# Kernel tuning notes

Measured on AMD Instinct MI355X. Metric: run time of the kernel, lower is better.

## Reference

```python
import jax, jax.numpy as jnp
import numpy as np

B, I, J, WIDTH, NH = 8, 1024, 1024, 512, 8
HD = WIDTH // NH
SCALE = WIDTH ** (-0.5)  # NOTE: original scales by width**-0.5, not head_dim**-0.5


def setup_inputs() -> dict:
    key = jax.random.key(0)
    ks = jax.random.split(key, 7)
    return {
        "q": jax.random.normal(ks[0], (B, I, WIDTH), dtype=jnp.float32),
        "k": jax.random.normal(ks[1], (B, J, WIDTH), dtype=jnp.float32),
        "v": jax.random.normal(ks[2], (B, J, WIDTH), dtype=jnp.float32),
        "Wq": jax.random.normal(ks[3], (WIDTH, WIDTH), dtype=jnp.float32) * (WIDTH ** -0.5),
        "Wk": jax.random.normal(ks[4], (WIDTH, WIDTH), dtype=jnp.float32) * (WIDTH ** -0.5),
        "Wv": jax.random.normal(ks[5], (WIDTH, WIDTH), dtype=jnp.float32) * (WIDTH ** -0.5),
        "Wo": jax.random.normal(ks[6], (WIDTH, WIDTH), dtype=jnp.float32) * (WIDTH ** -0.5),
    }


def reference(q, k, v, Wq, Wk, Wv, Wo):
    b, i, _ = q.shape
    j = k.shape[1]
    # Linear(bias=False): y = x @ W.T
    qh = (q @ Wq.T).reshape(b, NH, i, HD)  # faithful to torch .view(b, n, i, d) (no transpose)
    kh = (k @ Wk.T).reshape(b, NH, j, HD)
    vh = (v @ Wv.T).reshape(b, NH, j, HD)
    attn_score = jnp.einsum('bnid,bnjd->bnij', qh, kh) * SCALE
    attn_weight = jax.nn.softmax(attn_score, axis=3)
    # drop_prob = 0.0 -> dropout is identity
    x = jnp.einsum('bnij,bnjd->bnid', attn_weight, vh)
    x = x.transpose(0, 2, 1, 3).reshape(b, i, NH * HD)  # b n i d -> b i (n d)
    x = x @ Wo.T
    return (x, attn_weight)
```

## Files before the change

kernel.cpp:

```cpp
#include <hip/hip_runtime.h>
#include <hip/hip_bf16.h>


typedef __hip_bfloat16 bf16;
typedef __attribute__((ext_vector_type(8))) short bf16x8;
typedef __attribute__((ext_vector_type(4))) float f32x4;

#define BATCH 8
#define SEQ   1024
#define WIDTH 512
#define NHEAD 8
#define HD    64
#define SCALE_F 0.044194173824159216f

static __device__ __forceinline__ unsigned short f2bf(float x) {
  union { float f; unsigned u; } a; a.f = x;
  unsigned r = a.u + 0x7fffu + ((a.u >> 16) & 1u);
  return (unsigned short)(r >> 16);
}

static __device__ __forceinline__ void gload_lds16(const void* g, void* l) {
  __builtin_amdgcn_global_load_lds((const __attribute__((address_space(1))) void*)g,
                                   (__attribute__((address_space(3))) void*)l,
                                   16, 0, 0);
}

static __device__ __forceinline__ bf16x8 frag_ld(const short* tile, int row, int c16) {
  int p = c16 ^ (row & 7);
  return *(const bf16x8*)(tile + row*64 + p*8);
}

__global__ void cast_all_kernel(const float* __restrict__ q, const float* __restrict__ k,
                                const float* __restrict__ v, const float* __restrict__ wq,
                                const float* __restrict__ wk, const float* __restrict__ wv,
                                const float* __restrict__ wo, bf16* __restrict__ wsb) {
  const long NQ = 1048576;
  const long NW = 65536;
  long g = (long)blockIdx.x * blockDim.x + threadIdx.x;
  const float* src; bf16* dst; long o;
  if (g < 3*NQ) {
    int t = (int)(g / NQ); o = g - (long)t*NQ;
    src = (t==0) ? q : ((t==1) ? k : v);
    dst = wsb + (size_t)t * 4194304;
  } else {
    long g2 = g - 3*NQ;
    if (g2 >= 4*NW) return;
    int t = (int)(g2 / NW); o = g2 - (long)t*NW;
    src = (t==0) ? wq : ((t==1) ? wk : ((t==2) ? wv : wo));
    dst = wsb + (size_t)3*4194304 + (size_t)t * 262144;
  }
  float4 f = ((const float4*)src)[o];
  ushort4 r4;
  r4.x = f2bf(f.x); r4.y = f2bf(f.y); r4.z = f2bf(f.z); r4.w = f2bf(f.w);
  ((ushort4*)dst)[o] = r4;
}

template<int F32OUT, int NZ>
__global__ __launch_bounds__(256) void gemm_bt(const bf16* __restrict__ A0, const bf16* __restrict__ A1,
                                               const bf16* __restrict__ A2, const bf16* __restrict__ W0,
                                               const bf16* __restrict__ W1, const bf16* __restrict__ W2,
                                               void* __restrict__ C0, void* __restrict__ C1,
                                               void* __restrict__ C2) {
  __shared__ short As[2][128*64];
  __shared__ short Bs[2][128*64];

  const int bid = blockIdx.x;
  const int xcd = bid & 7;
  const int idx = bid >> 3;
  const int g   = xcd * (8*NZ) + (idx >> 2);
  const int y   = idx & 3;
  const int z   = g >> 6;
  const int m   = g & 63;

  const bf16* A; const bf16* Bw; void* Cout;
  if (NZ == 1 || z == 0) { A = A0; Bw = W0; Cout = C0; }
  else if (z == 1)       { A = A1; Bw = W1; Cout = C1; }
  else                   { A = A2; Bw = W2; Cout = C2; }

  const int lane = threadIdx.x & 63;
  const int wid  = threadIdx.x >> 6;
  const int m0 = m * 128;
  const int n0 = y * 128;
  const int wm = (wid >> 1) * 64;
  const int wn = (wid & 1) * 64;
  const int lrow = lane >> 3;
  const int swz  = ((lane & 7) ^ lrow) * 8;

  const f32x4 zero4 = {0.f,0.f,0.f,0.f};
  f32x4 acc[4][4];
  for (int i=0;i<4;++i) for (int j=0;j<4;++j) acc[i][j] = zero4;

  auto stage = [&](int buf, int t) {
    const int k0 = t * 64;
    for (int i = 0; i < 4; ++i) {
      int c = wid*4 + i;
      int row = c*8 + lrow;
      gload_lds16(A  + (size_t)(m0 + row)*WIDTH + k0 + swz, &As[buf][c*512]);
      gload_lds16(Bw + (size_t)(n0 + row)*WIDTH + k0 + swz, &Bs[buf][c*512]);
    }
  };

  stage(0, 0);
  asm volatile("s_waitcnt vmcnt(0)" ::: "memory");
  __syncthreads();
  int cur = 0;

  for (int t = 0; t < 8; ++t) {
    if (t < 7) stage(cur ^ 1, t + 1);
    for (int kc = 0; kc < 2; ++kc) {
      bf16x8 af[4], bfr[4];
      for (int mf=0; mf<4; ++mf) af[mf]  = frag_ld(&As[cur][0], wm + mf*16 + (lane&15), (lane>>4) + kc*4);
      for (int nf=0; nf<4; ++nf) bfr[nf] = frag_ld(&Bs[cur][0], wn + nf*16 + (lane&15), (lane>>4) + kc*4);
      for (int mf=0; mf<4; ++mf)
        for (int nf=0; nf<4; ++nf)
          acc[mf][nf] = __builtin_amdgcn_mfma_f32_16x16x32_bf16(af[mf], bfr[nf], acc[mf][nf], 0,0,0);
    }
    if (t < 7) {
      asm volatile("s_waitcnt vmcnt(0)" ::: "memory");
      __syncthreads();
      cur ^= 1;
    }
  }
  for (int mf=0; mf<4; ++mf)
    for (int nf=0; nf<4; ++nf) {
      int col = n0 + wn + nf*16 + (lane & 15);
      for (int r=0; r<4; ++r) {
        int row = m0 + wm + mf*16 + (lane>>4)*4 + r;
        if (F32OUT)
          ((float*)Cout)[(size_t)row*WIDTH + col] = acc[mf][nf][r];
        else
          ((unsigned short*)Cout)[(size_t)row*WIDTH + col] = f2bf(acc[mf][nf][r]);
      }
    }
}

__global__ __launch_bounds__(256) void transpose_v(const bf16* __restrict__ Vh,
                                                   bf16* __restrict__ Vt) {
  __shared__ short t[64][72];
  int h  = blockIdx.x >> 4;
  int j0 = (blockIdx.x & 15) * 64;
  const bf16* src = Vh + (size_t)h * (SEQ*HD);
  bf16* dst = Vt + (size_t)h * (SEQ*HD);
  int tid = threadIdx.x;
  int r  = tid >> 2;
  int c0 = (tid & 3) * 16;
  bf16x8 v0 = *(const bf16x8*)(src + (size_t)(j0 + r)*HD + c0);
  bf16x8 v1 = *(const bf16x8*)(src + (size_t)(j0 + r)*HD + c0 + 8);
  for (int i = 0; i < 8; ++i) { t[r][c0+i] = v0[i]; t[r][c0+8+i] = v1[i]; }
  __syncthreads();
  bf16x8 w0, w1;
  for (int i = 0; i < 8; ++i) { w0[i] = t[c0+i][r]; w1[i] = t[c0+8+i][r]; }
  *(bf16x8*)(dst + (size_t)r*SEQ + j0 + c0)     = w0;
  *(bf16x8*)(dst + (size_t)r*SEQ + j0 + c0 + 8) = w1;
}

__global__ __launch_bounds__(256) void attn_kernel(const bf16* __restrict__ Qh,
                                                   const bf16* __restrict__ Kh,
                                                   const bf16* __restrict__ Vt,
                                                   float* __restrict__ attn_out,
                                                   bf16* __restrict__ ctx) {
  __shared__ short Ks[2][64*64];
  __shared__ short Vs[2][64*64];
  __shared__ short Ws[4][16*64];

  const int lane = threadIdx.x & 63;
  const int wid  = threadIdx.x >> 6;
  const int bid  = blockIdx.x;
  const int xcd  = bid & 7;
  const int idx  = bid >> 3;
  const int h    = xcd*8 + (idx >> 4);
  const int i0   = (idx & 15) * 64;
  const int b  = h >> 3;
  const int nh = h & 7;

  const bf16* Qhead  = Qh + (size_t)h * (SEQ*HD);
  const bf16* Khead  = Kh + (size_t)h * (SEQ*HD);
  const bf16* Vthead = Vt + (size_t)h * (SEQ*HD);

  const int lrow = lane >> 3;
  const int swz  = ((lane & 7) ^ lrow) * 8;

  const int qrow = i0 + wid*16 + (lane & 15);
  bf16x8 qf[2];
  qf[0] = *(const bf16x8*)(Qhead + (size_t)qrow*HD + (lane>>4)*8);
  qf[1] = *(const bf16x8*)(Qhead + (size_t)qrow*HD + 32 + (lane>>4)*8);

  const f32x4 zero4 = {0.f,0.f,0.f,0.f};

  auto stageK = [&](int buf, int jt) {
    const int j0 = jt * 64;
    for (int i = 0; i < 2; ++i) {
      int c = wid*2 + i;
      gload_lds16(Khead + (size_t)(j0 + c*8 + lrow)*HD + swz, &Ks[buf][c*512]);
    }
  };
  auto stageV = [&](int buf, int jt) {
    const int j0 = jt * 64;
    for (int i = 0; i < 2; ++i) {
      int c = wid*2 + i;
      gload_lds16(Vthead + (size_t)(c*8 + lrow)*SEQ + j0 + swz, &Vs[buf][c*512]);
    }
  };

  float lsum[4] = {0.f,0.f,0.f,0.f};
  stageK(0, 0);
  asm volatile("s_waitcnt vmcnt(0)" ::: "memory");
  __syncthreads();
  int cur = 0;
  for (int jt = 0; jt < 16; ++jt) {
    if (jt < 15) stageK(cur ^ 1, jt + 1);
    f32x4 sac[4] = {zero4, zero4, zero4, zero4};
    __builtin_amdgcn_s_setprio(1);
    for (int kc = 0; kc < 2; ++kc)
      for (int jf = 0; jf < 4; ++jf) {
        bf16x8 kf = frag_ld(&Ks[cur][0], jf*16 + (lane & 15), (lane>>4) + kc*4);
        sac[jf] = __builtin_amdgcn_mfma_f32_16x16x32_bf16(qf[kc], kf, sac[jf], 0, 0, 0);
      }
    __builtin_amdgcn_s_setprio(0);
    for (int jf = 0; jf < 4; ++jf)
      for (int r = 0; r < 4; ++r)
        lsum[r] += __expf(sac[jf][r] * SCALE_F);
    if (jt < 15) {
      asm volatile("s_waitcnt vmcnt(0)" ::: "memory");
      __syncthreads();
      cur ^= 1;
    }
  }
  for (int m = 1; m < 16; m <<= 1)
    for (int r = 0; r < 4; ++r)
      lsum[r] += __shfl_xor(lsum[r], m, 64);
  float linv[4];
  for (int r = 0; r < 4; ++r) linv[r] = 1.0f / lsum[r];
  __syncthreads();

  f32x4 cacc[4] = {zero4, zero4, zero4, zero4};
  short* Wsw = &Ws[wid][0];
  stageK(0, 0); stageV(0, 0);
  asm volatile("s_waitcnt vmcnt(0)" ::: "memory");
  __syncthreads();
  cur = 0;
  for (int jt = 0; jt < 16; ++jt) {
    if (jt < 15) { stageK(cur ^ 1, jt + 1); stageV(cur ^ 1, jt + 1); }
    const int j0 = jt * 64;
    f32x4 sac[4] = {zero4, zero4, zero4, zero4};
    __builtin_amdgcn_s_setprio(1);
    for (int kc = 0; kc < 2; ++kc)
      for (int jf = 0; jf < 4; ++jf) {
        bf16x8 kf = frag_ld(&Ks[cur][0], jf*16 + (lane & 15), (lane>>4) + kc*4);
        sac[jf] = __builtin_amdgcn_mfma_f32_16x16x32_bf16(qf[kc], kf, sac[jf], 0, 0, 0);
      }
    __builtin_amdgcn_s_setprio(0);
    for (int jf = 0; jf < 4; ++jf)
      for (int r = 0; r < 4; ++r) {
        float w = __expf(sac[jf][r] * SCALE_F) * linv[r];
        int row = (lane>>4)*4 + r;
        int col = jf*16 + (lane & 15);
        attn_out[(size_t)(h*SEQ + i0 + wid*16 + row)*SEQ + j0 + col] = w;
        Wsw[row*64 + (((col>>3) ^ (row & 7))<<3) + (col & 7)] = (short)f2bf(w);
      }
    asm volatile("s_waitcnt lgkmcnt(0)" ::: "memory");
    __builtin_amdgcn_s_setprio(1);
    for (int kc = 0; kc < 2; ++kc) {
      bf16x8 wa = frag_ld(Wsw, lane & 15, (lane>>4) + kc*4);
      for (int df = 0; df < 4; ++df) {
        bf16x8 vb = frag_ld(&Vs[cur][0], df*16 + (lane & 15), (lane>>4) + kc*4);
        cacc[df] = __builtin_amdgcn_mfma_f32_16x16x32_bf16(wa, vb, cacc[df], 0, 0, 0);
      }
    }
    __builtin_amdgcn_s_setprio(0);
    if (jt < 15) {
      asm volatile("s_waitcnt vmcnt(0)" ::: "memory");
      __syncthreads();
      cur ^= 1;
    }
  }
  for (int df = 0; df < 4; ++df)
    for (int r = 0; r < 4; ++r) {
      int irow = i0 + wid*16 + (lane>>4)*4 + r;
      ((unsigned short*)ctx)[(size_t)(b*SEQ + irow)*WIDTH + nh*HD + df*16 + (lane & 15)]
          = f2bf(cacc[df][r]);
    }
}

extern "C" void kernel_launch(void* const* d_in, const int* in_sizes, int n_in,
                              void* d_out, int out_size, void* d_ws, size_t ws_size,
                              hipStream_t stream) {
  const float* q  = (const float*)d_in[0];
  const float* k  = (const float*)d_in[1];
  const float* v  = (const float*)d_in[2];
  const float* wq = (const float*)d_in[3];
  const float* wk = (const float*)d_in[4];
  const float* wv = (const float*)d_in[5];
  const float* wo = (const float*)d_in[6];

  bf16* wsb = (bf16*)d_ws;
  bf16* qb  = wsb;
  bf16* kb  = qb + 4194304;
  bf16* vb  = kb + 4194304;
  bf16* wqb = vb + 4194304;
  bf16* wkb = wqb + 262144;
  bf16* wvb = wkb + 262144;
  bf16* wob = wvb + 262144;
  bf16* Qh  = wob + 262144;
  bf16* Kh  = Qh + 4194304;
  bf16* Vh  = Kh + 4194304;
  bf16* Vt  = Vh + 4194304;
  bf16* ctx = Vt + 4194304;

  float* x_out    = (float*)d_out;
  float* attn_out = (float*)d_out + 4194304;

  cast_all_kernel<<<13312, 256, 0, stream>>>(q, k, v, wq, wk, wv, wo, wsb);
  gemm_bt<0,3><<<768, 256, 0, stream>>>(qb, kb, vb, wqb, wkb, wvb,
                                        (void*)Qh, (void*)Kh, (void*)Vh);
  transpose_v<<<1024, 256, 0, stream>>>(Vh, Vt);
  attn_kernel<<<1024, 256, 0, stream>>>(Qh, Kh, Vt, attn_out, ctx);
  gemm_bt<1,1><<<256, 256, 0, stream>>>(ctx, nullptr, nullptr, wob, nullptr, nullptr,
                                        (void*)x_out, nullptr, nullptr);
}
```

Baseline: 144.5 us.

## Fuse fp32-to-bf16 input cast into QKV GEMM and coalesce attention-weight stores

```diff
diff --git a/kernel.cpp b/kernel.cpp
--- a/kernel.cpp
+++ b/kernel.cpp
@@ -18,6 +18,9 @@
   unsigned r = a.u + 0x7fffu + ((a.u >> 16) & 1u);
   return (unsigned short)(r >> 16);
 }
+static __device__ __forceinline__ float bf2f(unsigned short u) {
+  union { unsigned u; float f; } a; a.u = ((unsigned)u) << 16; return a.f;
+}
 
 static __device__ __forceinline__ void gload_lds16(const void* g, void* l) {
   __builtin_amdgcn_global_load_lds((const __attribute__((address_space(1))) void*)g,
@@ -30,55 +33,45 @@
   return *(const bf16x8*)(tile + row*64 + p*8);
 }
 
-__global__ void cast_all_kernel(const float* __restrict__ q, const float* __restrict__ k,
-                                const float* __restrict__ v, const float* __restrict__ wq,
-                                const float* __restrict__ wk, const float* __restrict__ wv,
-                                const float* __restrict__ wo, bf16* __restrict__ wsb) {
-  const long NQ = 1048576;
+__global__ void wcast_kernel(const float* __restrict__ wq, const float* __restrict__ wk,
+                             const float* __restrict__ wv, const float* __restrict__ wo,
+                             bf16* __restrict__ wsb) {
   const long NW = 65536;
   long g = (long)blockIdx.x * blockDim.x + threadIdx.x;
-  const float* src; bf16* dst; long o;
-  if (g < 3*NQ) {
-    int t = (int)(g / NQ); o = g - (long)t*NQ;
-    src = (t==0) ? q : ((t==1) ? k : v);
-    dst = wsb + (size_t)t * 4194304;
-  } else {
-    long g2 = g - 3*NQ;
-    if (g2 >= 4*NW) return;
-    int t = (int)(g2 / NW); o = g2 - (long)t*NW;
-    src = (t==0) ? wq : ((t==1) ? wk : ((t==2) ? wv : wo));
-    dst = wsb + (size_t)3*4194304 + (size_t)t * 262144;
-  }
+  int t = (int)(g / NW); long o = g - (long)t*NW;
+  const float* src = (t==0) ? wq : ((t==1) ? wk : ((t==2) ? wv : wo));
+  bf16* dst = wsb + (size_t)t * 262144;
   float4 f = ((const float4*)src)[o];
   ushort4 r4;
   r4.x = f2bf(f.x); r4.y = f2bf(f.y); r4.z = f2bf(f.z); r4.w = f2bf(f.w);
   ((ushort4*)dst)[o] = r4;
 }
 
-template<int F32OUT, int NZ>
-__global__ __launch_bounds__(256) void gemm_bt(const bf16* __restrict__ A0, const bf16* __restrict__ A1,
-                                               const bf16* __restrict__ A2, const bf16* __restrict__ W0,
-                                               const bf16* __restrict__ W1, const bf16* __restrict__ W2,
-                                               void* __restrict__ C0, void* __restrict__ C1,
-                                               void* __restrict__ C2) {
+__global__ __launch_bounds__(256) void gemm_qkv(const float* __restrict__ Aq,
+                                                const float* __restrict__ Ak,
+                                                const float* __restrict__ Av,
+                                                const bf16* __restrict__ Wb,
+                                                bf16* __restrict__ Qh,
+                                                bf16* __restrict__ Kh,
+                                                bf16* __restrict__ Vh) {
   __shared__ short As[2][128*64];
   __shared__ short Bs[2][128*64];
 
   const int bid = blockIdx.x;
   const int xcd = bid & 7;
   const int idx = bid >> 3;
-  const int g   = xcd * (8*NZ) + (idx >> 2);
+  const int g   = xcd*24 + (idx >> 2);
   const int y   = idx & 3;
   const int z   = g >> 6;
   const int m   = g & 63;
 
-  const bf16* A; const bf16* Bw; void* Cout;
-  if (NZ == 1 || z == 0) { A = A0; Bw = W0; Cout = C0; }
-  else if (z == 1)       { A = A1; Bw = W1; Cout = C1; }
-  else                   { A = A2; Bw = W2; Cout = C2; }
+  const float* A = (z==0) ? Aq : ((z==1) ? Ak : Av);
+  const bf16* Bw = Wb + (size_t)z * 262144;
+  bf16* Cout = (z==0) ? Qh : ((z==1) ? Kh : Vh);
 
   const int lane = threadIdx.x & 63;
   const int wid  = threadIdx.x >> 6;
+  const int tid  = threadIdx.x;
   const int m0 = m * 128;
   const int n0 = y * 128;
   const int wm = (wid >> 1) * 64;
@@ -90,23 +83,45 @@
   f32x4 acc[4][4];
   for (int i=0;i<4;++i) for (int j=0;j<4;++j) acc[i][j] = zero4;
 
-  auto stage = [&](int buf, int t) {
+  float4 areg[8];
+  auto loadA = [&](int t) {
+    const int k0 = t * 64;
+    #pragma unroll
+    for (int s = 0; s < 8; ++s) {
+      int u = s*256 + tid;
+      int row = u >> 4, cu = u & 15;
+      areg[s] = *(const float4*)(A + (size_t)(m0 + row)*WIDTH + k0 + cu*4);
+    }
+  };
+  auto writeA = [&](int buf) {
+    #pragma unroll
+    for (int s = 0; s < 8; ++s) {
+      int u = s*256 + tid;
+      int row = u >> 4, cu = u & 15;
+      int lu = cu >> 1, half = cu & 1;
+      unsigned lo = (unsigned)f2bf(areg[s].x) | ((unsigned)f2bf(areg[s].y) << 16);
+      unsigned hi = (unsigned)f2bf(areg[s].z) | ((unsigned)f2bf(areg[s].w) << 16);
+      uint2 pk; pk.x = lo; pk.y = hi;
+      *(uint2*)(&As[buf][row*64 + ((lu ^ (row & 7)) << 3) + half*4]) = pk;
+    }
+  };
+  auto stageW = [&](int buf, int t) {
     const int k0 = t * 64;
     for (int i = 0; i < 4; ++i) {
       int c = wid*4 + i;
       int row = c*8 + lrow;
-      gload_lds16(A  + (size_t)(m0 + row)*WIDTH + k0 + swz, &As[buf][c*512]);
       gload_lds16(Bw + (size_t)(n0 + row)*WIDTH + k0 + swz, &Bs[buf][c*512]);
     }
   };
 
-  stage(0, 0);
+  loadA(0); stageW(0, 0);
   asm volatile("s_waitcnt vmcnt(0)" ::: "memory");
+  writeA(0);
   __syncthreads();
   int cur = 0;
 
   for (int t = 0; t < 8; ++t) {
-    if (t < 7) stage(cur ^ 1, t + 1);
+    if (t < 7) { stageW(cur ^ 1, t + 1); loadA(t + 1); }
     for (int kc = 0; kc < 2; ++kc) {
       bf16x8 af[4], bfr[4];
       for (int mf=0; mf<4; ++mf) af[mf]  = frag_ld(&As[cur][0], wm + mf*16 + (lane&15), (lane>>4) + kc*4);
@@ -117,19 +132,18 @@
     }
     if (t < 7) {
       asm volatile("s_waitcnt vmcnt(0)" ::: "memory");
+      writeA(cur ^ 1);
       __syncthreads();
       cur ^= 1;
     }
   }
+
   for (int mf=0; mf<4; ++mf)
     for (int nf=0; nf<4; ++nf) {
       int col = n0 + wn + nf*16 + (lane & 15);
       for (int r=0; r<4; ++r) {
         int row = m0 + wm + mf*16 + (lane>>4)*4 + r;
-        if (F32OUT)
-          ((float*)Cout)[(size_t)row*WIDTH + col] = acc[mf][nf][r];
-        else
-          ((unsigned short*)Cout)[(size_t)row*WIDTH + col] = f2bf(acc[mf][nf][r]);
+        ((unsigned short*)Cout)[(size_t)row*WIDTH + col] = f2bf(acc[mf][nf][r]);
       }
     }
 }
@@ -154,6 +168,72 @@
   *(bf16x8*)(dst + (size_t)r*SEQ + j0 + c0 + 8) = w1;
 }
 
+__global__ __launch_bounds__(256) void gemm_out(const bf16* __restrict__ A,
+                                                const bf16* __restrict__ Bw,
+                                                float* __restrict__ Cout) {
+  __shared__ short As[2][128*64];
+  __shared__ short Bs[2][128*64];
+
+  const int bid = blockIdx.x;
+  const int xcd = bid & 7;
+  const int idx = bid >> 3;
+  const int m   = xcd*8 + (idx >> 2);
+  const int y   = idx & 3;
+
+  const int lane = threadIdx.x & 63;
+  const int wid  = threadIdx.x >> 6;
+  const int m0 = m * 128;
+  const int n0 = y * 128;
+  const int wm = (wid >> 1) * 64;
+  const int wn = (wid & 1) * 64;
+  const int lrow = lane >> 3;
+  const int swz  = ((lane & 7) ^ lrow) * 8;
+
+  const f32x4 zero4 = {0.f,0.f,0.f,0.f};
+  f32x4 acc[4][4];
+  for (int i=0;i<4;++i) for (int j=0;j<4;++j) acc[i][j] = zero4;
+
+  auto stage = [&](int buf, int t) {
+    const int k0 = t * 64;
+    for (int i = 0; i < 4; ++i) {
+      int c = wid*4 + i;
+      int row = c*8 + lrow;
+      gload_lds16(A  + (size_t)(m0 + row)*WIDTH + k0 + swz, &As[buf][c*512]);
+      gload_lds16(Bw + (size_t)(n0 + row)*WIDTH + k0 + swz, &Bs[buf][c*512]);
+    }
+  };
+
+  stage(0, 0);
+  asm volatile("s_waitcnt vmcnt(0)" ::: "memory");
+  __syncthreads();
+  int cur = 0;
+
+  for (int t = 0; t < 8; ++t) {
+    if (t < 7) stage(cur ^ 1, t + 1);
+    for (int kc = 0; kc < 2; ++kc) {
+      bf16x8 af[4], bfr[4];
+      for (int mf=0; mf<4; ++mf) af[mf]  = frag_ld(&As[cur][0], wm + mf*16 + (lane&15), (lane>>4) + kc*4);
+      for (int nf=0; nf<4; ++nf) bfr[nf] = frag_ld(&Bs[cur][0], wn + nf*16 + (lane&15), (lane>>4) + kc*4);
+      for (int mf=0; mf<4; ++mf)
+        for (int nf=0; nf<4; ++nf)
+          acc[mf][nf] = __builtin_amdgcn_mfma_f32_16x16x32_bf16(af[mf], bfr[nf], acc[mf][nf], 0,0,0);
+    }
+    if (t < 7) {
+      asm volatile("s_waitcnt vmcnt(0)" ::: "memory");
+      __syncthreads();
+      cur ^= 1;
+    }
+  }
+  for (int mf=0; mf<4; ++mf)
+    for (int nf=0; nf<4; ++nf) {
+      int col = n0 + wn + nf*16 + (lane & 15);
+      for (int r=0; r<4; ++r) {
+        int row = m0 + wm + mf*16 + (lane>>4)*4 + r;
+        Cout[(size_t)row*WIDTH + col] = acc[mf][nf][r];
+      }
+    }
+}
+
 __global__ __launch_bounds__(256) void attn_kernel(const bf16* __restrict__ Qh,
                                                    const bf16* __restrict__ Kh,
                                                    const bf16* __restrict__ Vt,
@@ -235,6 +315,7 @@
 
   f32x4 cacc[4] = {zero4, zero4, zero4, zero4};
   short* Wsw = &Ws[wid][0];
+  float* awbase = attn_out + (size_t)((size_t)h*SEQ + i0 + wid*16)*SEQ;
   stageK(0, 0); stageV(0, 0);
   asm volatile("s_waitcnt vmcnt(0)" ::: "memory");
   __syncthreads();
@@ -255,7 +336,6 @@
         float w = __expf(sac[jf][r] * SCALE_F) * linv[r];
         int row = (lane>>4)*4 + r;
         int col = jf*16 + (lane & 15);
-        attn_out[(size_t)(h*SEQ + i0 + wid*16 + row)*SEQ + j0 + col] = w;
         Wsw[row*64 + (((col>>3) ^ (row & 7))<<3) + (col & 7)] = (short)f2bf(w);
       }
     asm volatile("s_waitcnt lgkmcnt(0)" ::: "memory");
@@ -268,9 +348,21 @@
       }
     }
     __builtin_amdgcn_s_setprio(0);
+    #pragma unroll
+    for (int s = 0; s < 4; ++s) {
+      int row = (lane>>4) + s*4;
+      int lu  = (lane & 15) >> 1;
+      uint2 pv = *(const uint2*)(Wsw + row*64 + ((lu ^ (row & 7)) << 3) + (lane & 1)*4);
+      float4 o;
+      o.x = bf2f((unsigned short)(pv.x & 0xffff));
+      o.y = bf2f((unsigned short)(pv.x >> 16));
+      o.z = bf2f((unsigned short)(pv.y & 0xffff));
+      o.w = bf2f((unsigned short)(pv.y >> 16));
+      *(float4*)(awbase + (size_t)row*SEQ + j0 + (lane & 15)*4) = o;
+    }
     if (jt < 15) {
-      asm volatile("s_waitcnt vmcnt(0)" ::: "memory");
-      __syncthreads();
+      asm volatile("s_waitcnt vmcnt(4) lgkmcnt(0)" ::: "memory");
+      __builtin_amdgcn_s_barrier();
       cur ^= 1;
     }
   }
@@ -294,14 +386,9 @@
   const float* wo = (const float*)d_in[6];
 
   bf16* wsb = (bf16*)d_ws;
-  bf16* qb  = wsb;
-  bf16* kb  = qb + 4194304;
-  bf16* vb  = kb + 4194304;
-  bf16* wqb = vb + 4194304;
-  bf16* wkb = wqb + 262144;
-  bf16* wvb = wkb + 262144;
-  bf16* wob = wvb + 262144;
-  bf16* Qh  = wob + 262144;
+  bf16* wqb = wsb;
+  bf16* wob = wqb + 3*262144;
+  bf16* Qh  = wqb + 4*262144;
   bf16* Kh  = Qh + 4194304;
   bf16* Vh  = Kh + 4194304;
   bf16* Vt  = Vh + 4194304;
@@ -310,11 +397,9 @@
   float* x_out    = (float*)d_out;
   float* attn_out = (float*)d_out + 4194304;
 
-  cast_all_kernel<<<13312, 256, 0, stream>>>(q, k, v, wq, wk, wv, wo, wsb);
-  gemm_bt<0,3><<<768, 256, 0, stream>>>(qb, kb, vb, wqb, wkb, wvb,
-                                        (void*)Qh, (void*)Kh, (void*)Vh);
+  wcast_kernel<<<1024, 256, 0, stream>>>(wq, wk, wv, wo, wqb);
+  gemm_qkv<<<768, 256, 0, stream>>>(q, k, v, wqb, Qh, Kh, Vh);
   transpose_v<<<1024, 256, 0, stream>>>(Vh, Vt);
   attn_kernel<<<1024, 256, 0, stream>>>(Qh, Kh, Vt, attn_out, ctx);
-  gemm_bt<1,1><<<256, 256, 0, stream>>>(ctx, nullptr, nullptr, wob, nullptr, nullptr,
-                                        (void*)x_out, nullptr, nullptr);
-}
+  gemm_out<<<256, 256, 0, stream>>>(ctx, wob, x_out);
+}
```

Result: slower. 154.9 us (+7.2%).
